# Performance work log

Hardware: AMD Instinct MI355X
Metric: run time of the kernel (lower is better)

Reference implementation:

```python
import jax, jax.numpy as jnp
import numpy as np

NEG_SLOPE = 0.2


def gat_conv(x, edge_src, edge_dst, W, att_src, att_dst, bias):
    """PyG-style GATConv (eval mode, concat=True, self-loops already appended).
    x: [N, F_in]; W: [F_in, H*C]; att_src/att_dst: [H, C]; bias: [H*C]."""
    N = x.shape[0]
    H, C = att_src.shape
    h = (x @ W).reshape(N, H, C)                      # [N,H,C]
    a_src = jnp.einsum('nhc,hc->nh', h, att_src)      # [N,H]
    a_dst = jnp.einsum('nhc,hc->nh', h, att_dst)      # [N,H]
    e = a_src[edge_src] + a_dst[edge_dst]             # [E',H]
    e = jax.nn.leaky_relu(e, NEG_SLOPE)
    # segment softmax over incoming edges per destination node
    e_max = jax.ops.segment_max(e, edge_dst, num_segments=N)   # [N,H]
    ex = jnp.exp(e - e_max[edge_dst])
    denom = jax.ops.segment_sum(ex, edge_dst, num_segments=N)  # [N,H]
    alpha = ex / denom[edge_dst]                       # [E',H]
    msg = h[edge_src] * alpha[:, :, None]              # [E',H,C]
    out = jax.ops.segment_sum(msg, edge_dst, num_segments=N)   # [N,H,C]
    return out.reshape(N, H * C) + bias


def setup_inputs() -> dict:
    key = jax.random.key(0)
    ks = jax.random.split(key, 16)
    N, E = 50000, 1600000
    x = jax.random.normal(ks[0], (N, 8), dtype=jnp.float32)
    edge_index = jax.random.randint(ks[1], (2, E), 0, N, dtype=jnp.int64)
    def glorot(k, shape):
        fan = sum(shape[-2:]) if len(shape) > 1 else shape[-1]
        return jax.random.normal(k, shape, dtype=jnp.float32) * (2.0 / fan) ** 0.5
    return {
        'x': x,
        'edge_index': edge_index,
        'W1': glorot(ks[2], (8, 32)),
        'att_src1': glorot(ks[3], (2, 16)),
        'att_dst1': glorot(ks[4], (2, 16)),
        'b1': jnp.zeros((32,), jnp.float32),
        'W2': glorot(ks[5], (32, 64)),
        'att_src2': glorot(ks[6], (2, 32)),
        'att_dst2': glorot(ks[7], (2, 32)),
        'b2': jnp.zeros((64,), jnp.float32),
        'fc1_w': glorot(ks[8], (64, 64)),
        'fc1_b': jnp.zeros((64,), jnp.float32),
        'fc2_w': glorot(ks[9], (64, 1)),
        'fc2_b': jnp.zeros((1,), jnp.float32),
    }


def reference(x, edge_index, W1, att_src1, att_dst1, b1, W2, att_src2, att_dst2, b2,
              fc1_w, fc1_b, fc2_w, fc2_b):
    N = x.shape[0]
    row, col = edge_index[0], edge_index[1]
    # GATConv adds self-loops internally (add_self_loops=True default)
    loops = jnp.arange(N, dtype=edge_index.dtype)
    src = jnp.concatenate([row, loops])
    dst = jnp.concatenate([col, loops])
    h = gat_conv(x, src, dst, W1, att_src1, att_dst1, b1)
    h = jax.nn.relu(h)
    h = gat_conv(h, src, dst, W2, att_src2, att_dst2, b2)
    h = jax.nn.relu(h)
    # edge-level head uses the ORIGINAL edge_index (no self-loops)
    e = h[row] + h[col]                                # [E,64]
    e = jax.nn.relu(e @ fc1_w + fc1_b)
    return e @ fc2_w + fc2_b                           # [E,1]
```

## Files before the change

kernel.cpp:

```cpp
#include <hip/hip_runtime.h>
#include <hip/hip_fp16.h>
#include <math.h>

#define NEG_SLOPE 0.2f
#define BKT_SHIFT 8
#define EPB 8192
#define MAXB 10240

__device__ __forceinline__ unsigned encf(float f) {
    unsigned u = __float_as_uint(f);
    return (u & 0x80000000u) ? ~u : (u | 0x80000000u);
}
__device__ __forceinline__ float decf(unsigned e) {
    unsigned u = (e & 0x80000000u) ? (e & 0x7FFFFFFFu) : ~e;
    return __uint_as_float(u);
}
__device__ __forceinline__ float lrelu(float t) { return fmaxf(t, NEG_SLOPE * t); }

__global__ void k_node1(const float* __restrict__ x, const float* __restrict__ W1,
                        const float* __restrict__ as1, const float* __restrict__ ad1,
                        __half* __restrict__ h1h, float* __restrict__ a_src1,
                        float* __restrict__ a_dst1, int N) {
    int n = blockIdx.x * blockDim.x + threadIdx.x;
    if (n >= N) return;
    float xv[8];
#pragma unroll
    for (int k = 0; k < 8; k++) xv[k] = x[n * 8 + k];
    float h[32];
#pragma unroll
    for (int j = 0; j < 32; j++) {
        float acc = 0.f;
#pragma unroll
        for (int k = 0; k < 8; k++) acc += xv[k] * W1[k * 32 + j];
        h[j] = acc;
        h1h[n * 32 + j] = __float2half(acc);
    }
#pragma unroll
    for (int hh = 0; hh < 2; hh++) {
        float s = 0.f, d = 0.f;
#pragma unroll
        for (int c = 0; c < 16; c++) {
            s += h[hh * 16 + c] * as1[hh * 16 + c];
            d += h[hh * 16 + c] * ad1[hh * 16 + c];
        }
        a_src1[n * 2 + hh] = s;
        a_dst1[n * 2 + hh] = d;
    }
}

__global__ void k_amax(const float* __restrict__ a, unsigned* __restrict__ outmax, int N) {
    int lane = threadIdx.x & 63;
    float mA = -1e30f, mB = -1e30f;
    for (int i = blockIdx.x * blockDim.x + threadIdx.x; i < N; i += gridDim.x * blockDim.x) {
        float2 v = *(const float2*)(a + 2 * (size_t)i);
        mA = fmaxf(mA, v.x); mB = fmaxf(mB, v.y);
    }
#pragma unroll
    for (int off = 32; off >= 1; off >>= 1) {
        mA = fmaxf(mA, __shfl_xor(mA, off));
        mB = fmaxf(mB, __shfl_xor(mB, off));
    }
    if (lane == 0) {
        atomicMax(&outmax[0], encf(mA));
        atomicMax(&outmax[1], encf(mB));
    }
}

__global__ __launch_bounds__(256) void k_bktA(const int* __restrict__ ei,
                                              int* __restrict__ bktCur,
                                              int2* __restrict__ bktbuf, int E, int K) {
    __shared__ int bh[256];
    __shared__ int bbase[256];
    __shared__ int loff[256];
    __shared__ int2 staged[EPB];
    __shared__ int gptr[EPB];
    int tid = threadIdx.x;
    int e0 = blockIdx.x * EPB;
    int e1 = e0 + EPB; if (e1 > E) e1 = E;
    int cnt = e1 - e0;
    bh[tid] = 0;
    __syncthreads();
    for (int i = e0 + tid; i < e1; i += 256)
        atomicAdd(&bh[ei[E + i] >> BKT_SHIFT], 1);
    __syncthreads();
    if (tid == 0) {
        int r = 0;
        for (int b = 0; b < K; b++) { loff[b] = r; r += bh[b]; }
    }
    if (tid < K) {
        int c = bh[tid];
        bbase[tid] = c > 0 ? atomicAdd(&bktCur[tid], c) : 0;
    }
    __syncthreads();
    bh[tid] = 0;
    __syncthreads();
    for (int i = e0 + tid; i < e1; i += 256) {
        int s = ei[i], d = ei[E + i];
        int b = d >> BKT_SHIFT, dl = d & 255;
        int r = atomicAdd(&bh[b], 1);
        int lp = loff[b] + r;
        staged[lp] = make_int2(s | (dl << 16), i);
        gptr[lp] = b * MAXB + bbase[b] + r;
    }
    __syncthreads();
    for (int i = tid; i < cnt; i += 256)
        bktbuf[gptr[i]] = staged[i];
}

__global__ void k_bktscan(const int* __restrict__ bktCur, int* __restrict__ bktOff, int K) {
    int lane = threadIdx.x;
    int chunk = (K + 63) >> 6;
    int beg = lane * chunk;
    int end = beg + chunk; if (end > K) end = K;
    int s = 0;
    for (int i = beg; i < end; i++) s += bktCur[i];
    int incl = s;
#pragma unroll
    for (int off = 1; off < 64; off <<= 1) {
        int v = __shfl_up(incl, off);
        if (lane >= off) incl += v;
    }
    int run = incl - s;
    for (int i = beg; i < end; i++) { bktOff[i] = run; run += bktCur[i]; }
    if (end == K) bktOff[K] = run;
}

__global__ __launch_bounds__(256) void k_bktB(const int* __restrict__ bktCur,
                                              const int* __restrict__ bktOff,
                                              const int2* __restrict__ bktbuf,
                                              int* __restrict__ rowp, int2* __restrict__ slotv,
                                              int N, int E, int K) {
    __shared__ int lhist[256];
    __shared__ int lrow[257];
    __shared__ int2 lslot[MAXB + 256];
    int k = blockIdx.x;
    int tid = threadIdx.x;
    int n0 = k << BKT_SHIFT;
    int nn = N - n0; if (nn > 256) nn = 256;
    int cnt = bktCur[k];
    int gbase = bktOff[k] + n0;
    lhist[tid] = 0;
    __syncthreads();
    const int2* rec = bktbuf + (size_t)k * MAXB;
    for (int i = tid; i < cnt; i += 256)
        atomicAdd(&lhist[(rec[i].x >> 16) & 255], 1);
    __syncthreads();
    if (tid == 0) {
        int r = 0;
        for (int i = 0; i < nn; i++) { lrow[i] = r; r += lhist[i] + 1; }
        lrow[nn] = r;
    }
    __syncthreads();
    if (tid < nn) {
        int lr = lrow[tid];
        rowp[n0 + tid] = gbase + lr;
        lslot[lr] = make_int2(n0 + tid, -1);
        lhist[tid] = lr + 1;
    }
    if (k == 0 && tid == 0) rowp[N] = E + N;
    __syncthreads();
    for (int i = tid; i < cnt; i += 256) {
        int2 rv = rec[i];
        int dl = (rv.x >> 16) & 255;
        int p = atomicAdd(&lhist[dl], 1);
        lslot[p] = make_int2(rv.x & 0xFFFF, rv.y);
    }
    __syncthreads();
    int tot = cnt + nn;
    for (int i = tid; i < tot; i += 256)
        slotv[gbase + i] = lslot[i];
}

__global__ __launch_bounds__(256) void k_conv1(
        const int* __restrict__ rowp, const int2* __restrict__ slotv,
        const float* __restrict__ a_src, const float* __restrict__ a_dst,
        const __half* __restrict__ h1h, const float* __restrict__ b1,
        const float* __restrict__ W2, const float* __restrict__ as2,
        const float* __restrict__ ad2,
        __half* __restrict__ h2h, float* __restrict__ a_src2,
        float* __restrict__ a_dst2, const unsigned* __restrict__ amax, int N) {
    __shared__ int   lsS[4][64];
    __shared__ float lsW[4][2][64];
    int tid = threadIdx.x;
    int lane = tid & 63;
    int wv = tid >> 6;
    int n = __builtin_amdgcn_readfirstlane((int)((blockIdx.x * blockDim.x + tid) >> 6));
    if (n >= N) return;
    int sub = lane & 31;
    int eslot = lane >> 5;
    int hh = sub >> 4;
    int beg = rowp[n], end = rowp[n + 1];
    float2 adv = *(const float2*)(a_dst + 2 * (size_t)n);
    float mA = lrelu(decf(amax[0]) + adv.x);
    float mB = lrelu(decf(amax[1]) + adv.y);
    float denom = 0.f, acc = 0.f;
    for (int j0 = beg; j0 < end; j0 += 64) {
        int idx = j0 + lane;
        bool valid = idx < end;
        int s = valid ? slotv[idx].x : 0;
        float2 as = valid ? *(const float2*)(a_src + 2 * (size_t)s)
                          : make_float2(0.f, 0.f);
        float tA = lrelu(as.x + adv.x);
        float tB = lrelu(as.y + adv.y);
        float wA = valid ? __expf(tA - mA) : 0.f;
        float wB = valid ? __expf(tB - mB) : 0.f;
        lsS[wv][lane] = s;
        lsW[wv][0][lane] = wA;
        lsW[wv][1][lane] = wB;
        float rA = wA, rB = wB;
#pragma unroll
        for (int off = 32; off >= 1; off >>= 1) {
            rA += __shfl_xor(rA, off);
            rB += __shfl_xor(rB, off);
        }
        denom += hh ? rB : rA;
        int cnt = end - j0; if (cnt > 64) cnt = 64;
#pragma unroll 4
        for (int jj = 0; jj < cnt; jj += 2) {
            int e = jj + eslot;
            int sj = lsS[wv][e];
            float wgt = lsW[wv][hh][e];
            acc += wgt * __half2float(h1h[sj * 32 + sub]);
        }
    }
    acc += __shfl_xor(acc, 32);
    float ov = fmaxf(acc / denom + b1[sub], 0.f);
    float acc2 = 0.f;
#pragma unroll
    for (int k = 0; k < 32; k++) acc2 += __shfl(ov, k, 32) * W2[k * 64 + lane];
    h2h[(size_t)n * 64 + lane] = __float2half(acc2);
    float p = acc2 * as2[lane];
    float q = acc2 * ad2[lane];
#pragma unroll
    for (int off = 16; off >= 1; off >>= 1) {
        p += __shfl_xor(p, off);
        q += __shfl_xor(q, off);
    }
    if ((lane & 31) == 0) {
        a_src2[n * 2 + (lane >> 5)] = p;
        a_dst2[n * 2 + (lane >> 5)] = q;
    }
}

__global__ __launch_bounds__(256) void k_conv2(
        const int* __restrict__ rowp, const int2* __restrict__ slotv,
        const float* __restrict__ a_src, const float* __restrict__ a_dst,
        const __half* __restrict__ h2h, const float* __restrict__ b2,
        const float* __restrict__ fw1, const float* __restrict__ fb1,
        __half* __restrict__ gh, const unsigned* __restrict__ amax, int N) {
    __shared__ int   lsS[4][64];
    __shared__ float lsW[4][2][64];
    int tid = threadIdx.x;
    int lane = tid & 63;
    int wv = tid >> 6;
    int n = __builtin_amdgcn_readfirstlane((int)((blockIdx.x * blockDim.x + tid) >> 6));
    if (n >= N) return;
    int hh = lane >> 5;
    int beg = rowp[n], end = rowp[n + 1];
    float2 adv = *(const float2*)(a_dst + 2 * (size_t)n);
    float mA = lrelu(decf(amax[0]) + adv.x);
    float mB = lrelu(decf(amax[1]) + adv.y);
    float denom = 0.f, acc = 0.f;
    for (int j0 = beg; j0 < end; j0 += 64) {
        int idx = j0 + lane;
        bool valid = idx < end;
        int s = valid ? slotv[idx].x : 0;
        float2 as = valid ? *(const float2*)(a_src + 2 * (size_t)s)
                          : make_float2(0.f, 0.f);
        float tA = lrelu(as.x + adv.x);
        float tB = lrelu(as.y + adv.y);
        float wA = valid ? __expf(tA - mA) : 0.f;
        float wB = valid ? __expf(tB - mB) : 0.f;
        lsS[wv][lane] = s;
        lsW[wv][0][lane] = wA;
        lsW[wv][1][lane] = wB;
        float rA = wA, rB = wB;
#pragma unroll
        for (int off = 32; off >= 1; off >>= 1) {
            rA += __shfl_xor(rA, off);
            rB += __shfl_xor(rB, off);
        }
        denom += hh ? rB : rA;
        int cnt = end - j0; if (cnt > 64) cnt = 64;
#pragma unroll 8
        for (int jj = 0; jj < cnt; jj++) {
            int sj = lsS[wv][jj];
            float wgt = lsW[wv][hh][jj];
            acc += wgt * __half2float(h2h[(size_t)sj * 64 + lane]);
        }
    }
    float res = fmaxf(acc / denom + b2[lane], 0.f);
    float gv = 0.5f * fb1[lane];
#pragma unroll
    for (int k = 0; k < 64; k++) gv += __shfl(res, k) * fw1[k * 64 + lane];
    gh[(size_t)n * 64 + lane] = __float2half(gv);
}

__global__ void k_head4(const int* __restrict__ rowp, const int2* __restrict__ slotv,
                        const __half* __restrict__ gh,
                        const float* __restrict__ w2, const float* __restrict__ b2,
                        float* __restrict__ out, int M, int N) {
    int t = blockIdx.x * blockDim.x + threadIdx.x;
    if (t >= M) return;
    int2 sv = slotv[t];
    int id = sv.y;
    if (id < 0) return;
    int lo = 0, hi = N;
    while (hi - lo > 1) {
        int mid = (lo + hi) >> 1;
        if (rowp[mid] <= t) lo = mid; else hi = mid;
    }
    int n = lo;
    int r = sv.x;
    const uint4* gr = (const uint4*)(gh + (size_t)r * 64);
    const uint4* gc = (const uint4*)(gh + (size_t)n * 64);
    float o = b2[0];
#pragma unroll
    for (int q = 0; q < 8; q++) {
        uint4 ua = gr[q], ub = gc[q];
#pragma unroll
        for (int w = 0; w < 4; w++) {
            unsigned a32 = (&ua.x)[w], b32 = (&ub.x)[w];
            float2 fa = __half22float2(*(const __half2*)&a32);
            float2 fb = __half22float2(*(const __half2*)&b32);
            int j = q * 8 + w * 2;
            o += fmaxf(fa.x + fb.x, 0.f) * w2[j];
            o += fmaxf(fa.y + fb.y, 0.f) * w2[j + 1];
        }
    }
    out[id] = o;
}

extern "C" void kernel_launch(void* const* d_in, const int* in_sizes, int n_in,
                              void* d_out, int out_size, void* d_ws, size_t ws_size,
                              hipStream_t stream) {
    const float* x   = (const float*)d_in[0];
    const int*   ei  = (const int*)d_in[1];
    const float* W1  = (const float*)d_in[2];
    const float* as1 = (const float*)d_in[3];
    const float* ad1 = (const float*)d_in[4];
    const float* b1  = (const float*)d_in[5];
    const float* W2  = (const float*)d_in[6];
    const float* as2 = (const float*)d_in[7];
    const float* ad2 = (const float*)d_in[8];
    const float* b2  = (const float*)d_in[9];
    const float* fw1 = (const float*)d_in[10];
    const float* fb1 = (const float*)d_in[11];
    const float* fw2 = (const float*)d_in[12];
    const float* fb2 = (const float*)d_in[13];
    float* out = (float*)d_out;

    int N = in_sizes[0] / 8;
    int E = in_sizes[1] / 2;
    int M = E + N;
    int K = (N + 255) >> BKT_SHIFT;

    float* h1slot = (float*)d_ws;
    float* asr1 = h1slot + (size_t)N * 32;
    float* adt1 = asr1 + (size_t)N * 2;
    float* out1 = adt1 + (size_t)N * 2;
    float* h2slot = out1 + (size_t)N * 32;
    float* asr2 = h2slot + (size_t)N * 64;
    float* adt2 = asr2 + (size_t)N * 2;
    int*   rowp = (int*)(adt2 + (size_t)N * 2);
    int2*  slotv = (int2*)(rowp + ((N + 2) & ~1));
    int*   bktCur = (int*)(slotv + M);
    unsigned* amax = (unsigned*)(bktCur + 256);
    int*   bktOff = (int*)(amax + 4);
    int2*  bktbuf = (int2*)out1;
    __half* h1h = (__half*)h1slot;
    __half* h2h = (__half*)h2slot;
    __half* gh  = (__half*)d_ws;

    int B = 256;
    k_node1<<<(N + B - 1) / B, B, 0, stream>>>(x, W1, as1, ad1, h1h, asr1, adt1, N);
    hipMemsetAsync(bktCur, 0, 260 * sizeof(int), stream);
    k_amax<<<64, 256, 0, stream>>>(asr1, amax, N);
    k_bktA<<<(E + EPB - 1) / EPB, 256, 0, stream>>>(ei, bktCur, bktbuf, E, K);
    k_bktscan<<<1, 64, 0, stream>>>(bktCur, bktOff, K);
    k_bktB<<<K, 256, 0, stream>>>(bktCur, bktOff, bktbuf, rowp, slotv, N, E, K);
    {
        long long thr = (long long)N * 64;
        k_conv1<<<(int)((thr + B - 1) / B), B, 0, stream>>>(rowp, slotv, asr1, adt1, h1h, b1,
                                                            W2, as2, ad2, h2h, asr2, adt2,
                                                            amax, N);
    }
    k_amax<<<64, 256, 0, stream>>>(asr2, amax + 2, N);
    {
        long long thr = (long long)N * 64;
        k_conv2<<<(int)((thr + B - 1) / B), B, 0, stream>>>(rowp, slotv, asr2, adt2, h2h, b2,
                                                            fw1, fb1, gh, amax + 2, N);
    }
    k_head4<<<(M + B - 1) / B, B, 0, stream>>>(rowp, slotv, gh, fw2, fb2, out, M, N);
}
```

Before: 242.8 us.

## Fuse layer-1 max into node kernel and vectorize half2 gathers in conv kernels

Folds the per-head maximum of the layer-1 source attention scores into k_node1 using a wave shuffle, a block reduction and an atomicMax, which removes the separate k_amax launch for layer 1 and the extra pass over a_src1. The conv1 and conv2 aggregation loops now load half2 pairs of features per lane and handle more edges per iteration (4 edges at once in conv1, 2 in conv2). This halves the gather instructions per edge and raises memory-level parallelism. The cost is extra cross-lane reductions and more bookkeeping with shuffles over paired channels.

```diff
diff --git a/kernel.cpp b/kernel.cpp
--- a/kernel.cpp
+++ b/kernel.cpp
@@ -17,34 +17,55 @@
 }
 __device__ __forceinline__ float lrelu(float t) { return fmaxf(t, NEG_SLOPE * t); }
 
-__global__ void k_node1(const float* __restrict__ x, const float* __restrict__ W1,
-                        const float* __restrict__ as1, const float* __restrict__ ad1,
-                        __half* __restrict__ h1h, float* __restrict__ a_src1,
-                        float* __restrict__ a_dst1, int N) {
-    int n = blockIdx.x * blockDim.x + threadIdx.x;
-    if (n >= N) return;
-    float xv[8];
-#pragma unroll
-    for (int k = 0; k < 8; k++) xv[k] = x[n * 8 + k];
-    float h[32];
-#pragma unroll
-    for (int j = 0; j < 32; j++) {
-        float acc = 0.f;
-#pragma unroll
-        for (int k = 0; k < 8; k++) acc += xv[k] * W1[k * 32 + j];
-        h[j] = acc;
-        h1h[n * 32 + j] = __float2half(acc);
-    }
-#pragma unroll
-    for (int hh = 0; hh < 2; hh++) {
-        float s = 0.f, d = 0.f;
-#pragma unroll
-        for (int c = 0; c < 16; c++) {
-            s += h[hh * 16 + c] * as1[hh * 16 + c];
-            d += h[hh * 16 + c] * ad1[hh * 16 + c];
-        }
-        a_src1[n * 2 + hh] = s;
-        a_dst1[n * 2 + hh] = d;
+__global__ __launch_bounds__(256) void k_node1(
+        const float* __restrict__ x, const float* __restrict__ W1,
+        const float* __restrict__ as1, const float* __restrict__ ad1,
+        __half* __restrict__ h1h, float* __restrict__ a_src1,
+        float* __restrict__ a_dst1, unsigned* __restrict__ amax, int N) {
+    __shared__ float wmax[4][2];
+    int tid = threadIdx.x;
+    int n = blockIdx.x * blockDim.x + tid;
+    float s0 = -1e30f, s1 = -1e30f;
+    if (n < N) {
+        float xv[8];
+#pragma unroll
+        for (int k = 0; k < 8; k++) xv[k] = x[n * 8 + k];
+        float h[32];
+#pragma unroll
+        for (int j = 0; j < 32; j++) {
+            float acc = 0.f;
+#pragma unroll
+            for (int k = 0; k < 8; k++) acc += xv[k] * W1[k * 32 + j];
+            h[j] = acc;
+            h1h[n * 32 + j] = __float2half(acc);
+        }
+        float sv[2];
+#pragma unroll
+        for (int hh = 0; hh < 2; hh++) {
+            float s = 0.f, d = 0.f;
+#pragma unroll
+            for (int c = 0; c < 16; c++) {
+                s += h[hh * 16 + c] * as1[hh * 16 + c];
+                d += h[hh * 16 + c] * ad1[hh * 16 + c];
+            }
+            a_src1[n * 2 + hh] = s;
+            a_dst1[n * 2 + hh] = d;
+            sv[hh] = s;
+        }
+        s0 = sv[0]; s1 = sv[1];
+    }
+#pragma unroll
+    for (int off = 32; off >= 1; off >>= 1) {
+        s0 = fmaxf(s0, __shfl_xor(s0, off));
+        s1 = fmaxf(s1, __shfl_xor(s1, off));
+    }
+    if ((tid & 63) == 0) { wmax[tid >> 6][0] = s0; wmax[tid >> 6][1] = s1; }
+    __syncthreads();
+    if (tid == 0) {
+        float m0 = fmaxf(fmaxf(wmax[0][0], wmax[1][0]), fmaxf(wmax[2][0], wmax[3][0]));
+        float m1 = fmaxf(fmaxf(wmax[0][1], wmax[1][1]), fmaxf(wmax[2][1], wmax[3][1]));
+        atomicMax(&amax[0], encf(m0));
+        atomicMax(&amax[1], encf(m1));
     }
 }
 
@@ -186,14 +207,15 @@
     int wv = tid >> 6;
     int n = __builtin_amdgcn_readfirstlane((int)((blockIdx.x * blockDim.x + tid) >> 6));
     if (n >= N) return;
-    int sub = lane & 31;
-    int eslot = lane >> 5;
-    int hh = sub >> 4;
+    int q = lane >> 4;
+    int c2 = lane & 15;
+    int hh = c2 >> 3;
     int beg = rowp[n], end = rowp[n + 1];
     float2 adv = *(const float2*)(a_dst + 2 * (size_t)n);
     float mA = lrelu(decf(amax[0]) + adv.x);
     float mB = lrelu(decf(amax[1]) + adv.y);
-    float denom = 0.f, acc = 0.f;
+    float denom = 0.f;
+    float accx = 0.f, accy = 0.f;
     for (int j0 = beg; j0 < end; j0 += 64) {
         int idx = j0 + lane;
         bool valid = idx < end;
@@ -216,29 +238,37 @@
         denom += hh ? rB : rA;
         int cnt = end - j0; if (cnt > 64) cnt = 64;
 #pragma unroll 4
-        for (int jj = 0; jj < cnt; jj += 2) {
-            int e = jj + eslot;
+        for (int jj = 0; jj < cnt; jj += 4) {
+            int e = jj + q;
             int sj = lsS[wv][e];
             float wgt = lsW[wv][hh][e];
-            acc += wgt * __half2float(h1h[sj * 32 + sub]);
-        }
-    }
-    acc += __shfl_xor(acc, 32);
-    float ov = fmaxf(acc / denom + b1[sub], 0.f);
+            __half2 f = *(const __half2*)(h1h + sj * 32 + 2 * c2);
+            float2 ff = __half22float2(f);
+            accx += wgt * ff.x;
+            accy += wgt * ff.y;
+        }
+    }
+    accx += __shfl_xor(accx, 16); accy += __shfl_xor(accy, 16);
+    accx += __shfl_xor(accx, 32); accy += __shfl_xor(accy, 32);
+    float ovx = fmaxf(accx / denom + b1[2 * c2], 0.f);
+    float ovy = fmaxf(accy / denom + b1[2 * c2 + 1], 0.f);
     float acc2 = 0.f;
 #pragma unroll
-    for (int k = 0; k < 32; k++) acc2 += __shfl(ov, k, 32) * W2[k * 64 + lane];
+    for (int p = 0; p < 16; p++) {
+        acc2 += __shfl(ovx, p) * W2[(2 * p) * 64 + lane];
+        acc2 += __shfl(ovy, p) * W2[(2 * p + 1) * 64 + lane];
+    }
     h2h[(size_t)n * 64 + lane] = __float2half(acc2);
     float p = acc2 * as2[lane];
-    float q = acc2 * ad2[lane];
+    float qd = acc2 * ad2[lane];
 #pragma unroll
     for (int off = 16; off >= 1; off >>= 1) {
         p += __shfl_xor(p, off);
-        q += __shfl_xor(q, off);
+        qd += __shfl_xor(qd, off);
     }
     if ((lane & 31) == 0) {
         a_src2[n * 2 + (lane >> 5)] = p;
-        a_dst2[n * 2 + (lane >> 5)] = q;
+        a_dst2[n * 2 + (lane >> 5)] = qd;
     }
 }
 
@@ -255,12 +285,15 @@
     int wv = tid >> 6;
     int n = __builtin_amdgcn_readfirstlane((int)((blockIdx.x * blockDim.x + tid) >> 6));
     if (n >= N) return;
-    int hh = lane >> 5;
+    int e2 = lane >> 5;
+    int c2 = lane & 31;
+    int hh = c2 >> 4;
     int beg = rowp[n], end = rowp[n + 1];
     float2 adv = *(const float2*)(a_dst + 2 * (size_t)n);
     float mA = lrelu(decf(amax[0]) + adv.x);
     float mB = lrelu(decf(amax[1]) + adv.y);
-    float denom = 0.f, acc = 0.f;
+    float denom = 0.f;
+    float accx = 0.f, accy = 0.f;
     for (int j0 = beg; j0 < end; j0 += 64) {
         int idx = j0 + lane;
         bool valid = idx < end;
@@ -283,16 +316,26 @@
         denom += hh ? rB : rA;
         int cnt = end - j0; if (cnt > 64) cnt = 64;
 #pragma unroll 8
-        for (int jj = 0; jj < cnt; jj++) {
-            int sj = lsS[wv][jj];
-            float wgt = lsW[wv][hh][jj];
-            acc += wgt * __half2float(h2h[(size_t)sj * 64 + lane]);
-        }
-    }
-    float res = fmaxf(acc / denom + b2[lane], 0.f);
+        for (int jj = 0; jj < cnt; jj += 2) {
+            int e = jj + e2;
+            int sj = lsS[wv][e];
+            float wgt = lsW[wv][hh][e];
+            __half2 f = *(const __half2*)(h2h + (size_t)sj * 64 + 2 * c2);
+            float2 ff = __half22float2(f);
+            accx += wgt * ff.x;
+            accy += wgt * ff.y;
+        }
+    }
+    accx += __shfl_xor(accx, 32);
+    accy += __shfl_xor(accy, 32);
+    float resx = fmaxf(accx / denom + b2[2 * c2], 0.f);
+    float resy = fmaxf(accy / denom + b2[2 * c2 + 1], 0.f);
     float gv = 0.5f * fb1[lane];
 #pragma unroll
-    for (int k = 0; k < 64; k++) gv += __shfl(res, k) * fw1[k * 64 + lane];
+    for (int p = 0; p < 32; p++) {
+        gv += __shfl(resx, p) * fw1[(2 * p) * 64 + lane];
+        gv += __shfl(resy, p) * fw1[(2 * p + 1) * 64 + lane];
+    }
     gh[(size_t)n * 64 + lane] = __float2half(gv);
 }
 
@@ -316,14 +359,14 @@
     const uint4* gc = (const uint4*)(gh + (size_t)n * 64);
     float o = b2[0];
 #pragma unroll
-    for (int q = 0; q < 8; q++) {
-        uint4 ua = gr[q], ub = gc[q];
+    for (int qq = 0; qq < 8; qq++) {
+        uint4 ua = gr[qq], ub = gc[qq];
 #pragma unroll
         for (int w = 0; w < 4; w++) {
             unsigned a32 = (&ua.x)[w], b32 = (&ub.x)[w];
             float2 fa = __half22float2(*(const __half2*)&a32);
             float2 fb = __half22float2(*(const __half2*)&b32);
-            int j = q * 8 + w * 2;
+            int j = qq * 8 + w * 2;
             o += fmaxf(fa.x + fb.x, 0.f) * w2[j];
             o += fmaxf(fa.y + fb.y, 0.f) * w2[j + 1];
         }
@@ -373,9 +416,8 @@
     __half* gh  = (__half*)d_ws;
 
     int B = 256;
-    k_node1<<<(N + B - 1) / B, B, 0, stream>>>(x, W1, as1, ad1, h1h, asr1, adt1, N);
     hipMemsetAsync(bktCur, 0, 260 * sizeof(int), stream);
-    k_amax<<<64, 256, 0, stream>>>(asr1, amax, N);
+    k_node1<<<(N + B - 1) / B, B, 0, stream>>>(x, W1, as1, ad1, h1h, asr1, adt1, amax, N);
     k_bktA<<<(E + EPB - 1) / EPB, 256, 0, stream>>>(ei, bktCur, bktbuf, E, K);
     k_bktscan<<<1, 64, 0, stream>>>(bktCur, bktOff, K);
     k_bktB<<<K, 256, 0, stream>>>(bktCur, bktOff, bktbuf, rowp, slotv, N, E, K);
```

Measured after the change: 237.5 us. 1.02x faster.
